# Optimization experiments

Measured on AMD Instinct MI355X. Metric: run time of the kernel, lower is better.

Reference implementation:

```python
import jax, jax.numpy as jnp
import numpy as np
import math

B, I, O = 512, 512, 512
MEXHAT_NORM = 2.0 / (math.sqrt(3.0) * math.pi ** 0.25)
BN_EPS = 1e-5


def setup_inputs() -> dict:
    key = jax.random.key(0)
    kx, kw = jax.random.split(key, 2)
    x = jax.random.normal(kx, (B, I), dtype=jnp.float32)
    scale = jnp.ones((I, O), dtype=jnp.float32)
    bias = jnp.zeros((I, O), dtype=jnp.float32)
    # kaiming_uniform_ with a=sqrt(5): bound = sqrt(6 / ((1 + a^2) * fan_in)) = 1/sqrt(fan_in)
    bound = 1.0 / math.sqrt(I)
    weight = jax.random.uniform(kw, (I, O), dtype=jnp.float32, minval=-bound, maxval=bound)
    # BatchNorm1d affine params
    gamma = jnp.ones((O,), dtype=jnp.float32)
    beta = jnp.zeros((O,), dtype=jnp.float32)
    return {"x": x, "scale": scale, "bias": bias, "weight": weight,
            "gamma": gamma, "beta": beta}


def _mexhat_kan(x, scale, bias, weight):
    # x: (B, I); scale/bias/weight: (I, O)
    t = (x[:, :, None] - bias[None, :, :]) / scale[None, :, :]      # (B, I, O)
    t2 = t * t
    wav = MEXHAT_NORM * (t2 - 1.0) * jnp.exp(-0.5 * t2)             # Mexican hat
    return jnp.einsum('bio,io->bo', wav, weight)                    # reduce over in_features


def _batchnorm_train(y, gamma, beta):
    # BatchNorm1d in training mode: biased batch statistics over the batch dim
    mean = jnp.mean(y, axis=0)
    var = jnp.mean((y - mean) ** 2, axis=0)
    return (y - mean) * jax.lax.rsqrt(var + BN_EPS) * gamma + beta


def reference(x, scale, bias, weight, gamma, beta):
    y = _mexhat_kan(x, scale, bias, weight)   # (B, O)
    return _batchnorm_train(y, gamma, beta)
```

## Files before the change

### kernel.cpp

```cpp
#include <hip/hip_runtime.h>
#include <math.h>

#define B_ 512
#define I_ 512
#define O_ 512
#define BO_ (B_*O_)
#define IO_ (I_*O_)

#define ZR 32
#define KIR 16

#define TB 64
#define TO 16
#define KI 16
#define ZN 8
#define NIZ (I_/ZN)
#define NCHZ (NIZ/KI)
#define LXS (TB + 4)
#define NCH (I_/KI)

#define SQH    0.84932180028801904f
#define MN_   (-1.2023679775792928f)
#define NN_   (-0.86732507058407750f)
#define BN_EPS (1e-5f)

#if defined(__has_builtin)
#if __has_builtin(__builtin_amdgcn_exp2f)
#define EXP2F(v) __builtin_amdgcn_exp2f(v)
#endif
#if __has_builtin(__builtin_amdgcn_global_load_lds)
#define HAVE_DMA 1
#endif
#endif
#ifndef EXP2F
#define EXP2F(v) exp2f(v)
#endif

#ifdef HAVE_DMA
__device__ __forceinline__ void dma16(const void* g, void* l) {
    __builtin_amdgcn_global_load_lds(
        (const __attribute__((address_space(1))) void*)g,
        (__attribute__((address_space(3))) void*)l, 16, 0, 0);
}
#endif

__global__ __launch_bounds__(256) void pack_px(
    const float* __restrict__ x, const float* __restrict__ scale,
    const float* __restrict__ bias, const float* __restrict__ weight,
    float4* __restrict__ pp, float* __restrict__ xT)
{
    const int bid = blockIdx.x;
    const int t   = threadIdx.x;

    if (bid < IO_ / 256) {
        const int g = bid * 256 + t;
        const float sc = scale[g];
        const float bi = bias[g];
        const float w  = weight[g];
        const float c  = SQH * __builtin_amdgcn_rcpf(sc);
        pp[g] = make_float4(c, -bi * c, MN_ * w, NN_ * w);
    } else {
        __shared__ float T[64][68];
        const int tile = bid - IO_ / 256;
        const int i0 = (tile & 7) * 64;
        const int b0 = (tile >> 3) * 64;
        const int r  = t >> 4;
        const int c4 = (t & 15) * 4;
        #pragma unroll
        for (int p = 0; p < 4; ++p) {
            const int b = b0 + r + p * 16;
            const float4 v = *reinterpret_cast<const float4*>(&x[(size_t)b * I_ + i0 + c4]);
            T[c4 + 0][r + p * 16] = v.x;
            T[c4 + 1][r + p * 16] = v.y;
            T[c4 + 2][r + p * 16] = v.z;
            T[c4 + 3][r + p * 16] = v.w;
        }
        __syncthreads();
        #pragma unroll
        for (int p = 0; p < 4; ++p) {
            const int il = r + p * 16;
            const float4 v = *reinterpret_cast<const float4*>(&T[il][c4]);
            *reinterpret_cast<float4*>(&xT[(size_t)(i0 + il) * B_ + b0 + c4]) = v;
        }
    }
}

#ifdef HAVE_DMA
__global__ __launch_bounds__(256) void kanR(
    const float4* __restrict__ pp, const float* __restrict__ xT,
    float* __restrict__ pY)
{
    __shared__ float4 Lp[KIR][64];
    __shared__ float  Lx[KIR][64];

    const int fid  = blockIdx.x;
    const int ot   = fid & 7;
    const int rest = fid >> 3;
    const int bt   = rest & 7;
    const int iz   = rest >> 3;

    const int o0 = ot * 64;
    const int b0 = bt * 64;
    const int i0 = iz * KIR;

    const int t  = threadIdx.x;
    const int oq = t & 15;
    const int bq = t >> 4;
    const int wv = t >> 6;
    const int l  = t & 63;

    #pragma unroll
    for (int k = 0; k < 4; ++k) {
        dma16(&pp[(size_t)(i0 + wv * 4 + k) * O_ + o0 + l],
              (char*)&Lp[0][0] + wv * 4096 + k * 1024);
    }
    dma16(&xT[(size_t)(i0 + wv * 4 + (l >> 4)) * B_ + b0 + (l & 15) * 4],
          (char*)&Lx[0][0] + wv * 1024);

    __syncthreads();

    float4 acc0 = {0,0,0,0}, acc1 = {0,0,0,0}, acc2 = {0,0,0,0}, acc3 = {0,0,0,0};

#define EVQ(xs, A)                                                           \
    {                                                                        \
        { const float h  = fmaf((xs), p0.x, p0.y);                           \
          const float un = -h * h;                                           \
          const float e  = EXP2F(un);                                        \
          const float gg = fmaf(un, p0.z, p0.w);                             \
          A.x = fmaf(gg, e, A.x); }                                          \
        { const float h  = fmaf((xs), p1.x, p1.y);                           \
          const float un = -h * h;                                           \
          const float e  = EXP2F(un);                                        \
          const float gg = fmaf(un, p1.z, p1.w);                             \
          A.y = fmaf(gg, e, A.y); }                                          \
        { const float h  = fmaf((xs), p2.x, p2.y);                           \
          const float un = -h * h;                                           \
          const float e  = EXP2F(un);                                        \
          const float gg = fmaf(un, p2.z, p2.w);                             \
          A.z = fmaf(gg, e, A.z); }                                          \
        { const float h  = fmaf((xs), p3.x, p3.y);                           \
          const float un = -h * h;                                           \
          const float e  = EXP2F(un);                                        \
          const float gg = fmaf(un, p3.z, p3.w);                             \
          A.w = fmaf(gg, e, A.w); }                                          \
    }

    #pragma unroll 4
    for (int ii = 0; ii < KIR; ++ii) {
        const float4 x4 = *reinterpret_cast<const float4*>(&Lx[ii][bq * 4]);
        const float4 p0 = Lp[ii][oq * 4 + 0];
        const float4 p1 = Lp[ii][oq * 4 + 1];
        const float4 p2 = Lp[ii][oq * 4 + 2];
        const float4 p3 = Lp[ii][oq * 4 + 3];
        EVQ(x4.x, acc0);
        EVQ(x4.y, acc1);
        EVQ(x4.z, acc2);
        EVQ(x4.w, acc3);
    }
#undef EVQ

    const size_t base = ((size_t)iz * B_ + b0 + bq * 4) * O_ + o0 + oq * 4;
    *reinterpret_cast<float4*>(&pY[base + 0 * O_]) = acc0;
    *reinterpret_cast<float4*>(&pY[base + 1 * O_]) = acc1;
    *reinterpret_cast<float4*>(&pY[base + 2 * O_]) = acc2;
    *reinterpret_cast<float4*>(&pY[base + 3 * O_]) = acc3;
}
#endif

__global__ __launch_bounds__(256) void kanZ(
    const float* __restrict__ x, const float* __restrict__ scale,
    const float* __restrict__ bias, const float* __restrict__ weight,
    float* __restrict__ pY)
{
    __shared__ float Lx[KI][LXS];
    __shared__ float Lp[KI][TO][4];

    const int fid = blockIdx.x;
    const int xcd = fid & 7;
    const int seq = fid >> 3;
    const int ot  = xcd * 4 + (seq & 3);
    const int by  = (seq >> 2) & 7;
    const int iz  = seq >> 5;

    const int o0 = ot * TO;
    const int b0 = by * TB;
    const int z0 = iz * NIZ;

    const int t   = threadIdx.x;
    const int to  = t & (TO - 1);
    const int tb4 = t >> 4;
    const int lb  = t >> 2;
    const int lq  = t & 3;
    const int li  = t >> 4;
    const int lo  = t & 15;

    float acc0 = 0.f, acc1 = 0.f, acc2 = 0.f, acc3 = 0.f;

    for (int ch = 0; ch < NCHZ; ++ch) {
        const int i0 = z0 + ch * KI;
        const float4 xv = *reinterpret_cast<const float4*>(
            &x[(size_t)(b0 + lb) * I_ + i0 + lq * 4]);
        const int pidx = (i0 + li) * O_ + o0 + lo;
        const float sc = scale[pidx];
        const float bi = bias[pidx];
        const float w  = weight[pidx];

        __syncthreads();
        Lx[lq * 4 + 0][lb] = xv.x;
        Lx[lq * 4 + 1][lb] = xv.y;
        Lx[lq * 4 + 2][lb] = xv.z;
        Lx[lq * 4 + 3][lb] = xv.w;
        const float c = SQH * __builtin_amdgcn_rcpf(sc);
        Lp[li][lo][0] = c;
        Lp[li][lo][1] = -bi * c;
        Lp[li][lo][2] = MN_ * w;
        Lp[li][lo][3] = NN_ * w;
        __syncthreads();

        #pragma unroll
        for (int ii = 0; ii < KI; ++ii) {
            const float4 p  = *reinterpret_cast<const float4*>(&Lp[ii][to][0]);
            const float4 x4 = *reinterpret_cast<const float4*>(&Lx[ii][tb4 * 4]);
            {
                const float h  = fmaf(x4.x, p.x, p.y);
                const float un = -h * h;
                const float e  = EXP2F(un);
                const float gg = fmaf(un, p.z, p.w);
                acc0 = fmaf(gg, e, acc0);
            }
            {
                const float h  = fmaf(x4.y, p.x, p.y);
                const float un = -h * h;
                const float e  = EXP2F(un);
                const float gg = fmaf(un, p.z, p.w);
                acc1 = fmaf(gg, e, acc1);
            }
            {
                const float h  = fmaf(x4.z, p.x, p.y);
                const float un = -h * h;
                const float e  = EXP2F(un);
                const float gg = fmaf(un, p.z, p.w);
                acc2 = fmaf(gg, e, acc2);
            }
            {
                const float h  = fmaf(x4.w, p.x, p.y);
                const float un = -h * h;
                const float e  = EXP2F(un);
                const float gg = fmaf(un, p.z, p.w);
                acc3 = fmaf(gg, e, acc3);
            }
        }
    }

    const size_t base = ((size_t)iz * B_ + b0 + tb4 * 4) * O_ + o0 + to;
    pY[base + 0 * O_] = acc0;
    pY[base + 1 * O_] = acc1;
    pY[base + 2 * O_] = acc2;
    pY[base + 3 * O_] = acc3;
}

template <int NZ>
__global__ __launch_bounds__(256) void comb_bn(
    const float* __restrict__ pY,
    const float* __restrict__ gamma, const float* __restrict__ beta,
    float* __restrict__ y)
{
    __shared__ float Ws[4][8];
    __shared__ float Ac[8];

    const int bid = blockIdx.x;
    const int o4  = (bid & 7) * 64 + (bid >> 3) * 4;
    const int t   = threadIdx.x;

    float4 v[2];
    float sx = 0.f, sy = 0.f, sz = 0.f, sw = 0.f;
    float qx = 0.f, qy = 0.f, qz = 0.f, qw = 0.f;
    #pragma unroll
    for (int r = 0; r < 2; ++r) {
        const int b = t + 256 * r;
        const size_t base = (size_t)b * O_ + o4;
        float4 a = *reinterpret_cast<const float4*>(&pY[base]);
        #pragma unroll
        for (int z = 1; z < NZ; ++z) {
            const float4 p = *reinterpret_cast<const float4*>(&pY[(size_t)z * BO_ + base]);
            a.x += p.x; a.y += p.y; a.z += p.z; a.w += p.w;
        }
        v[r] = a;
        sx += a.x; sy += a.y; sz += a.z; sw += a.w;
        qx += a.x * a.x; qy += a.y * a.y; qz += a.z * a.z; qw += a.w * a.w;
    }

    #pragma unroll
    for (int m = 1; m < 64; m <<= 1) {
        sx += __shfl_xor(sx, m); sy += __shfl_xor(sy, m);
        sz += __shfl_xor(sz, m); sw += __shfl_xor(sw, m);
        qx += __shfl_xor(qx, m); qy += __shfl_xor(qy, m);
        qz += __shfl_xor(qz, m); qw += __shfl_xor(qw, m);
    }
    if ((t & 63) == 0) {
        const int wv = t >> 6;
        Ws[wv][0] = sx; Ws[wv][1] = sy; Ws[wv][2] = sz; Ws[wv][3] = sw;
        Ws[wv][4] = qx; Ws[wv][5] = qy; Ws[wv][6] = qz; Ws[wv][7] = qw;
    }
    __syncthreads();
    if (t < 4) {
        const float s  = Ws[0][t]     + Ws[1][t]     + Ws[2][t]     + Ws[3][t];
        const float q  = Ws[0][t + 4] + Ws[1][t + 4] + Ws[2][t + 4] + Ws[3][t + 4];
        const float mean = s * (1.0f / B_);
        const float var  = q * (1.0f / B_) - mean * mean;
        const float inv  = rsqrtf(var + BN_EPS);
        const float a = gamma[o4 + t] * inv;
        Ac[t]     = a;
        Ac[t + 4] = fmaf(-mean, a, beta[o4 + t]);
    }
    __syncthreads();

    const float4 a4 = *reinterpret_cast<const float4*>(&Ac[0]);
    const float4 c4 = *reinterpret_cast<const float4*>(&Ac[4]);
    #pragma unroll
    for (int r = 0; r < 2; ++r) {
        const int b = t + 256 * r;
        float4 o;
        o.x = fmaf(v[r].x, a4.x, c4.x);
        o.y = fmaf(v[r].y, a4.y, c4.y);
        o.z = fmaf(v[r].z, a4.z, c4.z);
        o.w = fmaf(v[r].w, a4.w, c4.w);
        *reinterpret_cast<float4*>(&y[(size_t)b * O_ + o4]) = o;
    }
}


extern "C" void kernel_launch(void* const* d_in, const int* in_sizes, int n_in,
                              void* d_out, int out_size, void* d_ws, size_t ws_size,
                              hipStream_t stream) {
    const float* x      = (const float*)d_in[0];
    const float* scale  = (const float*)d_in[1];
    const float* bias   = (const float*)d_in[2];
    const float* weight = (const float*)d_in[3];
    const float* gamma  = (const float*)d_in[4];
    const float* beta   = (const float*)d_in[5];
    float* out = (float*)d_out;

    const size_t pYR_b = (size_t)ZR * BO_ * sizeof(float);
    const size_t pp_b  = (size_t)IO_ * sizeof(float4);
    const size_t xT_b  = (size_t)B_ * I_ * sizeof(float);
    const size_t needR = pYR_b + pp_b + xT_b;
    const size_t pYZ_b = (size_t)ZN * BO_ * sizeof(float);

#ifdef HAVE_DMA
    if (ws_size >= needR) {
        float*  pY = (float*)d_ws;
        float4* pp = (float4*)((char*)d_ws + pYR_b);
        float*  xT = (float*)((char*)d_ws + pYR_b + pp_b);

        pack_px<<<IO_ / 256 + 64, 256, 0, stream>>>(x, scale, bias, weight, pp, xT);
        kanR<<<8 * 8 * ZR, 256, 0, stream>>>(pp, xT, pY);
        comb_bn<ZR><<<O_ / 4, 256, 0, stream>>>(pY, gamma, beta, out);
        return;
    }
#endif
    if (ws_size >= pYZ_b) {
        float* pY = (float*)d_ws;
        kanZ<<<32 * 8 * 8, 256, 0, stream>>>(x, scale, bias, weight, pY);
        comb_bn<ZN><<<O_ / 4, 256, 0, stream>>>(pY, gamma, beta, out);
    }
}
```

Before: 33.05 us.

## Widen batch tile to 128 and swizzle packed params for conflict-free LDS reads

The main KAN kernel now covers 128 batch rows per block instead of 64, so each thread holds 8 accumulator rows and every parameter float4 loaded from LDS is reused across twice as many x values. The grid is halved to 1024 blocks. The packed per-(i,o) parameters are stored in a swizzled order so that threads read consecutive float4s instead of striding by 4, which is meant to avoid LDS bank conflicts. In exchange, registers per thread rise and fewer blocks are available for latency hiding.

```diff
diff --git a/kernel.cpp b/kernel.cpp
--- a/kernel.cpp
+++ b/kernel.cpp
@@ -7,8 +7,8 @@
 #define BO_ (B_*O_)
 #define IO_ (I_*O_)
 
-#define ZR 32
-#define KIR 16
+#define ZT 32
+#define KIT 16
 
 #define TB 64
 #define TO 16
@@ -17,7 +17,6 @@
 #define NIZ (I_/ZN)
 #define NCHZ (NIZ/KI)
 #define LXS (TB + 4)
-#define NCH (I_/KI)
 
 #define SQH    0.84932180028801904f
 #define MN_   (-1.2023679775792928f)
@@ -47,18 +46,23 @@
 __global__ __launch_bounds__(256) void pack_px(
     const float* __restrict__ x, const float* __restrict__ scale,
     const float* __restrict__ bias, const float* __restrict__ weight,
-    float4* __restrict__ pp, float* __restrict__ xT)
+    float4* __restrict__ ppS, float* __restrict__ xT)
 {
     const int bid = blockIdx.x;
     const int t   = threadIdx.x;
 
     if (bid < IO_ / 256) {
-        const int g = bid * 256 + t;
+        const int g  = bid * 256 + t;
+        const int i  = g >> 9;
+        const int o  = g & 511;
+        const int ot = o >> 6;
+        const int ol = o & 63;
         const float sc = scale[g];
         const float bi = bias[g];
         const float w  = weight[g];
         const float c  = SQH * __builtin_amdgcn_rcpf(sc);
-        pp[g] = make_float4(c, -bi * c, MN_ * w, NN_ * w);
+        const size_t idx = ((size_t)(i * 8 + ot) * 4 + (ol & 3)) * 16 + (ol >> 2);
+        ppS[idx] = make_float4(c, -bi * c, MN_ * w, NN_ * w);
     } else {
         __shared__ float T[64][68];
         const int tile = bid - IO_ / 256;
@@ -86,22 +90,21 @@
 }
 
 #ifdef HAVE_DMA
-__global__ __launch_bounds__(256) void kanR(
-    const float4* __restrict__ pp, const float* __restrict__ xT,
+__global__ __launch_bounds__(256) void kanT(
+    const float4* __restrict__ ppS, const float* __restrict__ xT,
     float* __restrict__ pY)
 {
-    __shared__ float4 Lp[KIR][64];
-    __shared__ float  Lx[KIR][64];
-
-    const int fid  = blockIdx.x;
-    const int ot   = fid & 7;
-    const int rest = fid >> 3;
-    const int bt   = rest & 7;
-    const int iz   = rest >> 3;
+    __shared__ float4 Lp[KIT][64];
+    __shared__ float  Lx[KIT][128];
+
+    const int fid = blockIdx.x;
+    const int ot  = fid & 7;
+    const int bt  = (fid >> 3) & 3;
+    const int iz  = fid >> 5;
 
     const int o0 = ot * 64;
-    const int b0 = bt * 64;
-    const int i0 = iz * KIR;
+    const int b0 = bt * 128;
+    const int i0 = iz * KIT;
 
     const int t  = threadIdx.x;
     const int oq = t & 15;
@@ -110,16 +113,21 @@
     const int l  = t & 63;
 
     #pragma unroll
-    for (int k = 0; k < 4; ++k) {
-        dma16(&pp[(size_t)(i0 + wv * 4 + k) * O_ + o0 + l],
-              (char*)&Lp[0][0] + wv * 4096 + k * 1024);
-    }
-    dma16(&xT[(size_t)(i0 + wv * 4 + (l >> 4)) * B_ + b0 + (l & 15) * 4],
-          (char*)&Lx[0][0] + wv * 1024);
+    for (int k4 = 0; k4 < 4; ++k4) {
+        dma16(&ppS[((size_t)(i0 + wv * 4 + k4) * 8 + ot) * 64 + l],
+              (char*)&Lp[0][0] + wv * 4096 + k4 * 1024);
+    }
+    #pragma unroll
+    for (int j = 0; j < 2; ++j) {
+        dma16(&xT[(size_t)(i0 + wv * 4 + j * 2 + (l >> 5)) * B_ + b0 + (l & 31) * 4],
+              (char*)&Lx[0][0] + wv * 2048 + j * 1024);
+    }
 
     __syncthreads();
 
-    float4 acc0 = {0,0,0,0}, acc1 = {0,0,0,0}, acc2 = {0,0,0,0}, acc3 = {0,0,0,0};
+    float4 a[8];
+    #pragma unroll
+    for (int r = 0; r < 8; ++r) a[r] = make_float4(0.f, 0.f, 0.f, 0.f);
 
 #define EVQ(xs, A)                                                           \
     {                                                                        \
@@ -145,25 +153,30 @@
           A.w = fmaf(gg, e, A.w); }                                          \
     }
 
-    #pragma unroll 4
-    for (int ii = 0; ii < KIR; ++ii) {
-        const float4 x4 = *reinterpret_cast<const float4*>(&Lx[ii][bq * 4]);
-        const float4 p0 = Lp[ii][oq * 4 + 0];
-        const float4 p1 = Lp[ii][oq * 4 + 1];
-        const float4 p2 = Lp[ii][oq * 4 + 2];
-        const float4 p3 = Lp[ii][oq * 4 + 3];
-        EVQ(x4.x, acc0);
-        EVQ(x4.y, acc1);
-        EVQ(x4.z, acc2);
-        EVQ(x4.w, acc3);
+    #pragma unroll 2
+    for (int ii = 0; ii < KIT; ++ii) {
+        const float4 p0 = Lp[ii][0 * 16 + oq];
+        const float4 p1 = Lp[ii][1 * 16 + oq];
+        const float4 p2 = Lp[ii][2 * 16 + oq];
+        const float4 p3 = Lp[ii][3 * 16 + oq];
+        const float4 xA = *reinterpret_cast<const float4*>(&Lx[ii][bq * 8 + 0]);
+        const float4 xB = *reinterpret_cast<const float4*>(&Lx[ii][bq * 8 + 4]);
+        EVQ(xA.x, a[0]);
+        EVQ(xA.y, a[1]);
+        EVQ(xA.z, a[2]);
+        EVQ(xA.w, a[3]);
+        EVQ(xB.x, a[4]);
+        EVQ(xB.y, a[5]);
+        EVQ(xB.z, a[6]);
+        EVQ(xB.w, a[7]);
     }
 #undef EVQ
 
-    const size_t base = ((size_t)iz * B_ + b0 + bq * 4) * O_ + o0 + oq * 4;
-    *reinterpret_cast<float4*>(&pY[base + 0 * O_]) = acc0;
-    *reinterpret_cast<float4*>(&pY[base + 1 * O_]) = acc1;
-    *reinterpret_cast<float4*>(&pY[base + 2 * O_]) = acc2;
-    *reinterpret_cast<float4*>(&pY[base + 3 * O_]) = acc3;
+    #pragma unroll
+    for (int r = 0; r < 8; ++r) {
+        const size_t base = ((size_t)iz * B_ + b0 + bq * 8 + r) * O_ + o0 + oq * 4;
+        *reinterpret_cast<float4*>(&pY[base]) = a[r];
+    }
 }
 #endif
 
@@ -341,21 +354,21 @@
     const float* beta   = (const float*)d_in[5];
     float* out = (float*)d_out;
 
-    const size_t pYR_b = (size_t)ZR * BO_ * sizeof(float);
+    const size_t pYT_b = (size_t)ZT * BO_ * sizeof(float);
     const size_t pp_b  = (size_t)IO_ * sizeof(float4);
     const size_t xT_b  = (size_t)B_ * I_ * sizeof(float);
-    const size_t needR = pYR_b + pp_b + xT_b;
+    const size_t needT = pYT_b + pp_b + xT_b;
     const size_t pYZ_b = (size_t)ZN * BO_ * sizeof(float);
 
 #ifdef HAVE_DMA
-    if (ws_size >= needR) {
-        float*  pY = (float*)d_ws;
-        float4* pp = (float4*)((char*)d_ws + pYR_b);
-        float*  xT = (float*)((char*)d_ws + pYR_b + pp_b);
-
-        pack_px<<<IO_ / 256 + 64, 256, 0, stream>>>(x, scale, bias, weight, pp, xT);
-        kanR<<<8 * 8 * ZR, 256, 0, stream>>>(pp, xT, pY);
-        comb_bn<ZR><<<O_ / 4, 256, 0, stream>>>(pY, gamma, beta, out);
+    if (ws_size >= needT) {
+        float*  pY  = (float*)d_ws;
+        float4* ppS = (float4*)((char*)d_ws + pYT_b);
+        float*  xT  = (float*)((char*)d_ws + pYT_b + pp_b);
+
+        pack_px<<<IO_ / 256 + 64, 256, 0, stream>>>(x, scale, bias, weight, ppS, xT);
+        kanT<<<8 * 4 * ZT, 256, 0, stream>>>(ppS, xT, pY);
+        comb_bn<ZT><<<O_ / 4, 256, 0, stream>>>(pY, gamma, beta, out);
         return;
     }
 #endif
```

New measurement: 32.91 us. About the same (-0.4%).

## Fuse parameter packing and x transpose into the main KAN kernel

Applied to the files above, without the earlier changes.

Removes the separate pack_px pre-pass and its workspace. The new kanW kernel loads scale, bias, weight and x tiles directly, computes the packed coefficients in registers, transposes x into LDS and then runs the same evaluation loop. This saves one kernel launch and the write and reread of packed parameters and transposed x. In exchange, each block recomputes its coefficient tile and uses plain loads instead of DMA to LDS, and since every (i,o) tile is read by 8 batch tiles, the coefficient work is repeated 8 times.

```diff
diff --git a/kernel.cpp b/kernel.cpp
--- a/kernel.cpp
+++ b/kernel.cpp
@@ -5,10 +5,8 @@
 #define I_ 512
 #define O_ 512
 #define BO_ (B_*O_)
-#define IO_ (I_*O_)
-
-#define ZR 32
-#define KIR 16
+
+#define ZW 32
 
 #define TB 64
 #define TO 16
@@ -17,7 +15,6 @@
 #define NIZ (I_/ZN)
 #define NCHZ (NIZ/KI)
 #define LXS (TB + 4)
-#define NCH (I_/KI)
 
 #define SQH    0.84932180028801904f
 #define MN_   (-1.2023679775792928f)
@@ -27,99 +24,70 @@
 #if defined(__has_builtin)
 #if __has_builtin(__builtin_amdgcn_exp2f)
 #define EXP2F(v) __builtin_amdgcn_exp2f(v)
-#endif
-#if __has_builtin(__builtin_amdgcn_global_load_lds)
-#define HAVE_DMA 1
 #endif
 #endif
 #ifndef EXP2F
 #define EXP2F(v) exp2f(v)
 #endif
 
-#ifdef HAVE_DMA
-__device__ __forceinline__ void dma16(const void* g, void* l) {
-    __builtin_amdgcn_global_load_lds(
-        (const __attribute__((address_space(1))) void*)g,
-        (__attribute__((address_space(3))) void*)l, 16, 0, 0);
-}
-#endif
-
-__global__ __launch_bounds__(256) void pack_px(
+__global__ __launch_bounds__(256) void kanW(
     const float* __restrict__ x, const float* __restrict__ scale,
     const float* __restrict__ bias, const float* __restrict__ weight,
-    float4* __restrict__ pp, float* __restrict__ xT)
-{
-    const int bid = blockIdx.x;
-    const int t   = threadIdx.x;
-
-    if (bid < IO_ / 256) {
-        const int g = bid * 256 + t;
-        const float sc = scale[g];
-        const float bi = bias[g];
-        const float w  = weight[g];
-        const float c  = SQH * __builtin_amdgcn_rcpf(sc);
-        pp[g] = make_float4(c, -bi * c, MN_ * w, NN_ * w);
-    } else {
-        __shared__ float T[64][68];
-        const int tile = bid - IO_ / 256;
-        const int i0 = (tile & 7) * 64;
-        const int b0 = (tile >> 3) * 64;
-        const int r  = t >> 4;
-        const int c4 = (t & 15) * 4;
-        #pragma unroll
-        for (int p = 0; p < 4; ++p) {
-            const int b = b0 + r + p * 16;
-            const float4 v = *reinterpret_cast<const float4*>(&x[(size_t)b * I_ + i0 + c4]);
-            T[c4 + 0][r + p * 16] = v.x;
-            T[c4 + 1][r + p * 16] = v.y;
-            T[c4 + 2][r + p * 16] = v.z;
-            T[c4 + 3][r + p * 16] = v.w;
-        }
-        __syncthreads();
-        #pragma unroll
-        for (int p = 0; p < 4; ++p) {
-            const int il = r + p * 16;
-            const float4 v = *reinterpret_cast<const float4*>(&T[il][c4]);
-            *reinterpret_cast<float4*>(&xT[(size_t)(i0 + il) * B_ + b0 + c4]) = v;
-        }
-    }
-}
-
-#ifdef HAVE_DMA
-__global__ __launch_bounds__(256) void kanR(
-    const float4* __restrict__ pp, const float* __restrict__ xT,
     float* __restrict__ pY)
 {
-    __shared__ float4 Lp[KIR][64];
-    __shared__ float  Lx[KIR][64];
-
-    const int fid  = blockIdx.x;
-    const int ot   = fid & 7;
-    const int rest = fid >> 3;
-    const int bt   = rest & 7;
-    const int iz   = rest >> 3;
+    __shared__ float4 Lp[16][4][16];
+    __shared__ float  Lx[16][64];
+
+    const int fid = blockIdx.x;
+    const int ot  = fid & 7;
+    const int bt  = (fid >> 3) & 7;
+    const int iz  = fid >> 6;
 
     const int o0 = ot * 64;
     const int b0 = bt * 64;
-    const int i0 = iz * KIR;
-
-    const int t  = threadIdx.x;
-    const int oq = t & 15;
-    const int bq = t >> 4;
-    const int wv = t >> 6;
-    const int l  = t & 63;
-
-    #pragma unroll
-    for (int k = 0; k < 4; ++k) {
-        dma16(&pp[(size_t)(i0 + wv * 4 + k) * O_ + o0 + l],
-              (char*)&Lp[0][0] + wv * 4096 + k * 1024);
-    }
-    dma16(&xT[(size_t)(i0 + wv * 4 + (l >> 4)) * B_ + b0 + (l & 15) * 4],
-          (char*)&Lx[0][0] + wv * 1024);
+    const int i0 = iz * 16;
+
+    const int t   = threadIdx.x;
+    const int oq  = t & 15;
+    const int bq  = t >> 4;
+    const int si  = t >> 4;
+    const int so4 = t & 15;
+    const int lb  = t >> 2;
+    const int lq  = t & 3;
+
+    {
+        const size_t g = (size_t)(i0 + si) * O_ + o0 + so4 * 4;
+        const float4 s4 = *reinterpret_cast<const float4*>(&scale[g]);
+        const float4 b4 = *reinterpret_cast<const float4*>(&bias[g]);
+        const float4 w4 = *reinterpret_cast<const float4*>(&weight[g]);
+        const float4 xv = *reinterpret_cast<const float4*>(
+            &x[(size_t)(b0 + lb) * I_ + i0 + lq * 4]);
+
+        {
+            const float c = SQH * __builtin_amdgcn_rcpf(s4.x);
+            Lp[si][0][so4] = make_float4(c, -b4.x * c, MN_ * w4.x, NN_ * w4.x);
+        }
+        {
+            const float c = SQH * __builtin_amdgcn_rcpf(s4.y);
+            Lp[si][1][so4] = make_float4(c, -b4.y * c, MN_ * w4.y, NN_ * w4.y);
+        }
+        {
+            const float c = SQH * __builtin_amdgcn_rcpf(s4.z);
+            Lp[si][2][so4] = make_float4(c, -b4.z * c, MN_ * w4.z, NN_ * w4.z);
+        }
+        {
+            const float c = SQH * __builtin_amdgcn_rcpf(s4.w);
+            Lp[si][3][so4] = make_float4(c, -b4.w * c, MN_ * w4.w, NN_ * w4.w);
+        }
+        Lx[lq * 4 + 0][lb] = xv.x;
+        Lx[lq * 4 + 1][lb] = xv.y;
+        Lx[lq * 4 + 2][lb] = xv.z;
+        Lx[lq * 4 + 3][lb] = xv.w;
+    }
 
     __syncthreads();
 
-    float4 acc0 = {0,0,0,0}, acc1 = {0,0,0,0}, acc2 = {0,0,0,0}, acc3 = {0,0,0,0};
+    float4 a0 = {0,0,0,0}, a1 = {0,0,0,0}, a2 = {0,0,0,0}, a3 = {0,0,0,0};
 
 #define EVQ(xs, A)                                                           \
     {                                                                        \
@@ -146,26 +114,25 @@
     }
 
     #pragma unroll 4
-    for (int ii = 0; ii < KIR; ++ii) {
+    for (int ii = 0; ii < 16; ++ii) {
+        const float4 p0 = Lp[ii][0][oq];
+        const float4 p1 = Lp[ii][1][oq];
+        const float4 p2 = Lp[ii][2][oq];
+        const float4 p3 = Lp[ii][3][oq];
         const float4 x4 = *reinterpret_cast<const float4*>(&Lx[ii][bq * 4]);
-        const float4 p0 = Lp[ii][oq * 4 + 0];
-        const float4 p1 = Lp[ii][oq * 4 + 1];
-        const float4 p2 = Lp[ii][oq * 4 + 2];
-        const float4 p3 = Lp[ii][oq * 4 + 3];
-        EVQ(x4.x, acc0);
-        EVQ(x4.y, acc1);
-        EVQ(x4.z, acc2);
-        EVQ(x4.w, acc3);
+        EVQ(x4.x, a0);
+        EVQ(x4.y, a1);
+        EVQ(x4.z, a2);
+        EVQ(x4.w, a3);
     }
 #undef EVQ
 
     const size_t base = ((size_t)iz * B_ + b0 + bq * 4) * O_ + o0 + oq * 4;
-    *reinterpret_cast<float4*>(&pY[base + 0 * O_]) = acc0;
-    *reinterpret_cast<float4*>(&pY[base + 1 * O_]) = acc1;
-    *reinterpret_cast<float4*>(&pY[base + 2 * O_]) = acc2;
-    *reinterpret_cast<float4*>(&pY[base + 3 * O_]) = acc3;
+    *reinterpret_cast<float4*>(&pY[base + 0 * O_]) = a0;
+    *reinterpret_cast<float4*>(&pY[base + 1 * O_]) = a1;
+    *reinterpret_cast<float4*>(&pY[base + 2 * O_]) = a2;
+    *reinterpret_cast<float4*>(&pY[base + 3 * O_]) = a3;
 }
-#endif
 
 __global__ __launch_bounds__(256) void kanZ(
     const float* __restrict__ x, const float* __restrict__ scale,
@@ -341,25 +308,14 @@
     const float* beta   = (const float*)d_in[5];
     float* out = (float*)d_out;
 
-    const size_t pYR_b = (size_t)ZR * BO_ * sizeof(float);
-    const size_t pp_b  = (size_t)IO_ * sizeof(float4);
-    const size_t xT_b  = (size_t)B_ * I_ * sizeof(float);
-    const size_t needR = pYR_b + pp_b + xT_b;
+    const size_t pYW_b = (size_t)ZW * BO_ * sizeof(float);
     const size_t pYZ_b = (size_t)ZN * BO_ * sizeof(float);
 
-#ifdef HAVE_DMA
-    if (ws_size >= needR) {
-        float*  pY = (float*)d_ws;
-        float4* pp = (float4*)((char*)d_ws + pYR_b);
-        float*  xT = (float*)((char*)d_ws + pYR_b + pp_b);
-
-        pack_px<<<IO_ / 256 + 64, 256, 0, stream>>>(x, scale, bias, weight, pp, xT);
-        kanR<<<8 * 8 * ZR, 256, 0, stream>>>(pp, xT, pY);
-        comb_bn<ZR><<<O_ / 4, 256, 0, stream>>>(pY, gamma, beta, out);
-        return;
-    }
-#endif
-    if (ws_size >= pYZ_b) {
+    if (ws_size >= pYW_b) {
+        float* pY = (float*)d_ws;
+        kanW<<<8 * 8 * ZW, 256, 0, stream>>>(x, scale, bias, weight, pY);
+        comb_bn<ZW><<<O_ / 4, 256, 0, stream>>>(pY, gamma, beta, out);
+    } else if (ws_size >= pYZ_b) {
         float* pY = (float*)d_ws;
         kanZ<<<32 * 8 * 8, 256, 0, stream>>>(x, scale, bias, weight, pY);
         comb_bn<ZN><<<O_ / 4, 256, 0, stream>>>(pY, gamma, beta, out);
```

Measured after the change: 49.53 us. 1.5x slower.
